# Kernel tuning notes

Hardware: AMD Instinct MI355X
Metric: run time of the kernel (lower is better)

Reference implementation:

```python
import jax, jax.numpy as jnp
import numpy as np
import math

D_MODEL = 1024
N_HEADS = 16
D_K = D_MODEL // N_HEADS
BSZ = 4
SEQ = 2048


def setup_inputs() -> dict:
    key = jax.random.key(0)
    ks = jax.random.split(key, 10)
    x = jax.random.normal(ks[0], (BSZ, SEQ, D_MODEL), dtype=jnp.float32)
    pad_mask = jnp.zeros((BSZ, 1, 1, SEQ), dtype=jnp.int32)
    s = 0.02
    Wq = jax.random.normal(ks[1], (D_MODEL, D_MODEL), jnp.float32) * s
    bq = jax.random.normal(ks[2], (D_MODEL,), jnp.float32) * s
    Wk = jax.random.normal(ks[3], (D_MODEL, D_MODEL), jnp.float32) * s
    bk = jax.random.normal(ks[4], (D_MODEL,), jnp.float32) * s
    Wv = jax.random.normal(ks[5], (D_MODEL, D_MODEL), jnp.float32) * s
    bv = jax.random.normal(ks[6], (D_MODEL,), jnp.float32) * s
    Wo = jax.random.normal(ks[7], (D_MODEL, D_MODEL), jnp.float32) * s
    bo = jax.random.normal(ks[8], (D_MODEL,), jnp.float32) * s
    return {"x": x, "pad_mask": pad_mask, "Wq": Wq, "bq": bq, "Wk": Wk,
            "bk": bk, "Wv": Wv, "bv": bv, "Wo": Wo, "bo": bo}


def reference(x, pad_mask, Wq, bq, Wk, bk, Wv, bv, Wo, bo):
    bsz, seq_len, d_model = x.shape
    h, dk = N_HEADS, D_K

    def split(W, b):
        # torch Linear: x @ W.T + b ; then [b,s,h,dk] -> [b,h,s,dk]
        y = jnp.einsum('bsd,ed->bse', x, W) + b
        return y.reshape(bsz, seq_len, h, dk).transpose(0, 2, 1, 3)

    q = split(Wq, bq)
    k = split(Wk, bk)
    v = split(Wv, bv)

    scores = jnp.einsum('bhqd,bhkd->bhqk', q, k) / math.sqrt(dk)
    causal = jnp.triu(jnp.ones((seq_len, seq_len), dtype=bool), k=1)
    scores = jnp.where(causal[None, None], -jnp.inf, scores)
    scores = jnp.where(pad_mask == 1, -jnp.inf, scores)
    attn = jax.nn.softmax(scores, axis=-1)
    attn = jnp.nan_to_num(attn, nan=0.0)
    out = jnp.einsum('bhqk,bhkd->bhqd', attn, v)
    out = out.transpose(0, 2, 1, 3).reshape(bsz, seq_len, d_model)
    # dropout is identity in eval mode
    return jnp.einsum('bsd,ed->bse', out, Wo) + bo
```

## Files before the change

kernel.cpp:

```cpp
#include <hip/hip_runtime.h>
#include <stdint.h>
#include <stddef.h>


typedef __bf16 bf16;
typedef __bf16 bf16x8 __attribute__((ext_vector_type(8)));
typedef __bf16 bf16x4 __attribute__((ext_vector_type(4)));
typedef float f32x4 __attribute__((ext_vector_type(4)));

#define DM   1024
#define NH   16
#define DK   64
#define BSZ  4
#define SEQL 2048
#define NTOK 8192
#define NEGB -3.0e38f

__device__ __forceinline__ void async16(const bf16* g, void* l) {
  __builtin_amdgcn_global_load_lds(
      (__attribute__((address_space(1))) void*)g,
      (__attribute__((address_space(3))) void*)l, 16, 0, 0);
}

__global__ __launch_bounds__(256) void cvt_all(
    const float* __restrict__ x,
    const float* __restrict__ w0, const float* __restrict__ w1,
    const float* __restrict__ w2, const float* __restrict__ w3,
    const int* __restrict__ pad,
    bf16* __restrict__ xd,
    bf16* __restrict__ d0, bf16* __restrict__ d1,
    bf16* __restrict__ d2, bf16* __restrict__ d3,
    float* __restrict__ padf) {
  int blk = blockIdx.x;
  if (blk >= 6144) {
    int i = (blk - 6144) * 2048 + threadIdx.x * 8;
    int4 p0 = *(const int4*)(pad + i);
    int4 p1 = *(const int4*)(pad + i + 4);
    float4 o0 = {p0.x ? NEGB : 0.f, p0.y ? NEGB : 0.f, p0.z ? NEGB : 0.f, p0.w ? NEGB : 0.f};
    float4 o1 = {p1.x ? NEGB : 0.f, p1.y ? NEGB : 0.f, p1.z ? NEGB : 0.f, p1.w ? NEGB : 0.f};
    *(float4*)(padf + i) = o0;
    *(float4*)(padf + i + 4) = o1;
    return;
  }
  const float* s; bf16* d; int i;
  if (blk < 4096) { s = x; d = xd; i = blk * 2048 + threadIdx.x * 8; }
  else {
    int m = (blk - 4096) >> 9, bi = (blk - 4096) & 511;
    switch (m) {
      case 0:  s = w0; d = d0; break;
      case 1:  s = w1; d = d1; break;
      case 2:  s = w2; d = d2; break;
      default: s = w3; d = d3; break;
    }
    i = bi * 2048 + threadIdx.x * 8;
  }
  float4 v0 = *(const float4*)(s + i);
  float4 v1 = *(const float4*)(s + i + 4);
  bf16x8 o = {(bf16)v0.x, (bf16)v0.y, (bf16)v0.z, (bf16)v0.w,
              (bf16)v1.x, (bf16)v1.y, (bf16)v1.z, (bf16)v1.w};
  *(bf16x8*)(d + i) = o;
}

template <int OUT_MODE>
__device__ __forceinline__ void gemm_core(const bf16* __restrict__ A,
                                          const bf16* __restrict__ W,
                                          const float* __restrict__ bias,
                                          void* __restrict__ outp,
                                          int bm, int bn, char* smem) {
  const int tid  = threadIdx.x;
  const int lane = tid & 63;
  const int wv   = tid >> 6;
  const int wr   = wv >> 2;
  const int wc   = wv & 3;
  const int c    = lane & 15;
  const int quad = lane >> 4;

  const int sr = tid >> 3;
  const int sj = ((tid & 7) ^ (sr & 7)) << 3;
  const bf16* gA = A + (size_t)(bm + sr) * DM + sj;
  const bf16* gB = W + (size_t)(bn + sr) * DM + sj;

#define STAGE_A(TT, TGT) {                                        \
    char* la_ = smem + (TGT) * 49152 + tid * 16;                  \
    async16(gA + (size_t)(TT) * 64, la_);                         \
    async16(gA + (size_t)64 * DM + (size_t)(TT) * 64, la_ + 8192); }
#define STAGE_B(TT, TGT) {                                        \
    char* lb_ = smem + (TGT) * 49152 + 16384 + tid * 16;          \
    async16(gB + (size_t)(TT) * 64, lb_);                         \
    async16(gB + (size_t)64 * DM + (size_t)(TT) * 64, lb_ + 8192);  \
    async16(gB + (size_t)128 * DM + (size_t)(TT) * 64, lb_ + 16384); \
    async16(gB + (size_t)192 * DM + (size_t)(TT) * 64, lb_ + 24576); }

  int aoff[2][4], boff[2][4];
#pragma unroll
  for (int kk = 0; kk < 2; ++kk) {
    const int sw = ((kk * 4 + quad) ^ (c & 7)) << 4;
#pragma unroll
    for (int i = 0; i < 4; ++i) {
      aoff[kk][i] = (wr * 64 + i * 16 + c) * 128 + sw;
      boff[kk][i] = 16384 + (wc * 64 + i * 16 + c) * 128 + sw;
    }
  }

  f32x4 acc[4][4] = {};

  STAGE_A(0, 0) STAGE_B(0, 0)
  STAGE_A(1, 1) STAGE_B(1, 1)
  asm volatile("s_waitcnt vmcnt(6)" ::: "memory");
  __builtin_amdgcn_s_barrier();
  __builtin_amdgcn_sched_barrier(0);

#pragma unroll
  for (int T = 0; T < 16; ++T) {
    const char* bufc = smem + (T % 3) * 49152;
    const int TGT = (T + 2) % 3;
    bf16x8 a0[4], b0[4], a1[4], b1[4];
#pragma unroll
    for (int i = 0; i < 4; ++i) a0[i] = *(const bf16x8*)(bufc + aoff[0][i]);
#pragma unroll
    for (int i = 0; i < 4; ++i) b0[i] = *(const bf16x8*)(bufc + boff[0][i]);
    __builtin_amdgcn_sched_barrier(0);
#pragma unroll
    for (int i = 0; i < 4; ++i) a1[i] = *(const bf16x8*)(bufc + aoff[1][i]);
#pragma unroll
    for (int i = 0; i < 4; ++i) b1[i] = *(const bf16x8*)(bufc + boff[1][i]);
    if (T < 14) { STAGE_A(T + 2, TGT) STAGE_B(T + 2, TGT) }
    __builtin_amdgcn_s_barrier();
    asm volatile("s_waitcnt lgkmcnt(8)" ::: "memory");
    __builtin_amdgcn_sched_barrier(0);
    __builtin_amdgcn_s_setprio(1);
#pragma unroll
    for (int mi = 0; mi < 4; ++mi)
#pragma unroll
      for (int ni = 0; ni < 4; ++ni)
        acc[mi][ni] = __builtin_amdgcn_mfma_f32_16x16x32_bf16(a0[mi], b0[ni],
                                                              acc[mi][ni], 0, 0, 0);
    __builtin_amdgcn_s_setprio(0);
    asm volatile("s_waitcnt lgkmcnt(0)" ::: "memory");
    __builtin_amdgcn_sched_barrier(0);
    __builtin_amdgcn_s_setprio(1);
#pragma unroll
    for (int mi = 0; mi < 4; ++mi)
#pragma unroll
      for (int ni = 0; ni < 4; ++ni)
        acc[mi][ni] = __builtin_amdgcn_mfma_f32_16x16x32_bf16(a1[mi], b1[ni],
                                                              acc[mi][ni], 0, 0, 0);
    __builtin_amdgcn_s_setprio(0);
    if (T < 14)       asm volatile("s_waitcnt vmcnt(6)" ::: "memory");
    else if (T == 14) asm volatile("s_waitcnt vmcnt(0)" ::: "memory");
    __builtin_amdgcn_s_barrier();
    __builtin_amdgcn_sched_barrier(0);
  }
#undef STAGE_A
#undef STAGE_B

  float bias_r[4];
#pragma unroll
  for (int ni = 0; ni < 4; ++ni) bias_r[ni] = bias[bn + wc * 64 + ni * 16 + c];

  if constexpr (OUT_MODE == 2) {
    __syncthreads();
    bf16* vt = (bf16*)smem + wv * 4608;
#pragma unroll
    for (int mi = 0; mi < 4; ++mi)
#pragma unroll
      for (int ni = 0; ni < 4; ++ni) {
        bf16x4 pv = {(bf16)(acc[mi][ni][0] + bias_r[ni]),
                     (bf16)(acc[mi][ni][1] + bias_r[ni]),
                     (bf16)(acc[mi][ni][2] + bias_r[ni]),
                     (bf16)(acc[mi][ni][3] + bias_r[ni])};
        *(bf16x4*)&vt[(ni * 16 + c) * 72 + mi * 16 + quad * 4] = pv;
      }
    const int base = bm + wr * 64;
    const int bb = base >> 11, s0 = base & 2047;
    const int rl = lane >> 3, cl = lane & 7;
#pragma unroll
    for (int it = 0; it < 8; ++it) {
      int d_row = it * 8 + rl;
      bf16x8 v = *(const bf16x8*)&vt[d_row * 72 + cl * 8];
      int n_g = bn + wc * 64 + d_row;
      int hh = n_g >> 6, dd = n_g & 63;
      *(bf16x8*)&((bf16*)outp)[(((size_t)(bb * NH + hh)) * DK + dd) * SEQL + s0 + cl * 8] = v;
    }
    return;
  }

#pragma unroll
  for (int mi = 0; mi < 4; ++mi) {
#pragma unroll
    for (int reg = 0; reg < 4; ++reg) {
      int m_g = bm + wr * 64 + mi * 16 + quad * 4 + reg;
#pragma unroll
      for (int ni = 0; ni < 4; ++ni) {
        int n_g = bn + wc * 64 + ni * 16 + c;
        float v = acc[mi][ni][reg] + bias_r[ni];
        if (OUT_MODE == 0) {
          int b = m_g >> 11, s = m_g & 2047;
          int h = n_g >> 6, d = n_g & 63;
          ((bf16*)outp)[(((size_t)(b * NH + h) * SEQL + s) << 6) + d] = (bf16)v;
        } else {
          ((float*)outp)[(size_t)m_g * DM + n_g] = v;
        }
      }
    }
  }
}

__global__ __launch_bounds__(512, 2) void qkv_gemm(
    const bf16* __restrict__ X,
    const bf16* __restrict__ Wq, const bf16* __restrict__ Wk, const bf16* __restrict__ Wv,
    const float* __restrict__ bq, const float* __restrict__ bk, const float* __restrict__ bv,
    bf16* __restrict__ Q, bf16* __restrict__ K, bf16* __restrict__ Vt) {
  __shared__ alignas(16) char smem[147456];
  const int f = blockIdx.x;
  const int wg = (f & 7) * 96 + (f >> 3);
  const int y = wg / 12, t = wg % 12;
  const int z = t >> 2, x = t & 3;
  const int bm = y * 128, bn = x * 256;
  if (z < 2)
    gemm_core<0>(X, z ? Wk : Wq, z ? bk : bq, z ? (void*)K : (void*)Q, bm, bn, smem);
  else
    gemm_core<2>(X, Wv, bv, Vt, bm, bn, smem);
}

__global__ __launch_bounds__(512, 2) void out_gemm(const bf16* __restrict__ A,
                                                   const bf16* __restrict__ W,
                                                   const float* __restrict__ bias,
                                                   float* __restrict__ out) {
  __shared__ alignas(16) char smem[147456];
  const int f = blockIdx.x;
  const int wg = (f & 7) * 32 + (f >> 3);
  gemm_core<1>(A, W, bias, out, (wg >> 2) * 128, (wg & 3) * 256, smem);
}

__global__ __launch_bounds__(512, 2) void attn_kernel(
    const bf16* __restrict__ Q, const bf16* __restrict__ K,
    const bf16* __restrict__ Vt, const float* __restrict__ padf,
    bf16* __restrict__ O) {
  const int B = blockIdx.x;
  const int bh = (B & 7) + 8 * (B >> 5);
  const int t  = (B >> 3) & 3;
  const int b = bh >> 4, h = bh & 15;
  const int tid  = threadIdx.x;
  const int lane = tid & 63;
  const int wv   = tid >> 6;
  const int c    = lane & 15;
  const int quad = lane >> 4;

  __shared__ bf16 Ks[2][64 * 64];
  __shared__ bf16 Vs[2][64 * 64];
  __shared__ bf16 Pl_all[8][32 * 64];
  bf16* Pl = &Pl_all[wv][0];

  const bf16* Qh  = Q  + (size_t)bh * SEQL * DK;
  const bf16* Kh  = K  + (size_t)bh * SEQL * DK;
  const bf16* Vth = Vt + (size_t)bh * DK * SEQL;
  const float* pb = padf + b * SEQL;

  const int sr = tid >> 3;
  const int sj = ((tid & 7) ^ (sr & 7)) * 8;
  const bf16* gK = Kh  + (size_t)sr * DK   + sj;
  const bf16* gV = Vth + (size_t)sr * SEQL + sj;
  bf16* lK0 = &Ks[0][tid * 8]; bf16* lK1 = &Ks[1][tid * 8];
  bf16* lV0 = &Vs[0][tid * 8]; bf16* lV1 = &Vs[1][tid * 8];

  const float sc = 0.1803368801111204f;

  for (int pass = 0; pass < 2; ++pass) {
    const int qt  = pass ? 7 - t : t;
    const int R   = qt * 256 + wv * 32;
    const int nkt = (qt + 1) * 4;

    bf16x8 Qf[2][2];
#pragma unroll
    for (int qg = 0; qg < 2; ++qg)
#pragma unroll
      for (int kh = 0; kh < 2; ++kh)
        Qf[qg][kh] = *(const bf16x8*)&Qh[(size_t)(R + qg * 16 + c) * DK + kh * 32 + quad * 8];

    f32x4 Oc[2][4] = {};
    float ls[2] = {0.f, 0.f};

    __syncthreads();
    async16(gK, lK0);
    async16(gV, lV0);

    for (int kt = 0; kt < nkt; ++kt) {
      const int cur = kt & 1;
      const int kb = kt * 64;
      __syncthreads();

      if (kt + 1 < nkt) {
        async16(gK + (size_t)(kt + 1) * 64 * DK, cur ? lK0 : lK1);
        async16(gV + (size_t)(kt + 1) * 64,      cur ? lV0 : lV1);
      }
      if (kb > R + 31) continue;

      float4 bc[4];
#pragma unroll
      for (int kf = 0; kf < 4; ++kf)
        bc[kf] = *(const float4*)&pb[kb + kf * 16 + quad * 4];

      const bf16* Kc = cur ? Ks[1] : Ks[0];
      const bf16* Vc = cur ? Vs[1] : Vs[0];

      bf16x8 Kf[4][2], Vf[4][2];
#pragma unroll
      for (int kf = 0; kf < 4; ++kf)
#pragma unroll
        for (int kh = 0; kh < 2; ++kh)
          Kf[kf][kh] = *(const bf16x8*)&Kc[(kf * 16 + c) * 64 + (((kh * 4 + quad) ^ (c & 7)) * 8)];
#pragma unroll
      for (int df = 0; df < 4; ++df)
#pragma unroll
        for (int kv = 0; kv < 2; ++kv)
          Vf[df][kv] = *(const bf16x8*)&Vc[(df * 16 + c) * 64 + (((kv * 4 + quad) ^ (c & 7)) * 8)];

      f32x4 st[2][4] = {};
#pragma unroll
      for (int qg = 0; qg < 2; ++qg)
#pragma unroll
        for (int kh = 0; kh < 2; ++kh)
#pragma unroll
          for (int kf = 0; kf < 4; ++kf)
            st[qg][kf] = __builtin_amdgcn_mfma_f32_16x16x32_bf16(Kf[kf][kh], Qf[qg][kh],
                                                                 st[qg][kf], 0, 0, 0);

      const bool dg = (kb + 63 > R);
#pragma unroll
      for (int qg = 0; qg < 2; ++qg) {
        const int qrow = R + qg * 16 + c;
#pragma unroll
        for (int kf = 0; kf < 4; ++kf) {
          const float* bv4 = (const float*)&bc[kf];
          float p4[4];
#pragma unroll
          for (int r = 0; r < 4; ++r) {
            float e = __builtin_amdgcn_exp2f(__builtin_fmaf(st[qg][kf][r], sc, bv4[r]));
            if (dg && (kb + kf * 16 + quad * 4 + r > qrow)) e = 0.f;
            p4[r] = e;
            ls[qg] += e;
          }
          bf16x4 pk = {(bf16)p4[0], (bf16)p4[1], (bf16)p4[2], (bf16)p4[3]};
          *(bf16x4*)&Pl[(qg * 16 + c) * 64 +
                        (((kf * 2 + (quad >> 1)) ^ (c & 7)) * 8) + (quad & 1) * 4] = pk;
        }
      }

#pragma unroll
      for (int qg = 0; qg < 2; ++qg)
#pragma unroll
        for (int kv = 0; kv < 2; ++kv) {
          bf16x8 af = *(const bf16x8*)&Pl[(qg * 16 + c) * 64 +
                                          (((kv * 4 + quad) ^ (c & 7)) * 8)];
#pragma unroll
          for (int df = 0; df < 4; ++df)
            Oc[qg][df] = __builtin_amdgcn_mfma_f32_16x16x32_bf16(af, Vf[df][kv],
                                                                 Oc[qg][df], 0, 0, 0);
        }
    }

#pragma unroll
    for (int qg = 0; qg < 2; ++qg) {
      float l = ls[qg];
      l += __shfl_xor(l, 16);
      l += __shfl_xor(l, 32);
      float linv = (l > 0.f) ? 1.f / l : 0.f;
      float lr[4];
#pragma unroll
      for (int r = 0; r < 4; ++r) lr[r] = __shfl(linv, quad * 4 + r);
#pragma unroll
      for (int r = 0; r < 4; ++r) {
        size_t row = (size_t)(b * SEQL + R + qg * 16 + quad * 4 + r) * DM + h * DK;
#pragma unroll
        for (int df = 0; df < 4; ++df)
          O[row + df * 16 + c] = (bf16)(Oc[qg][df][r] * lr[r]);
      }
    }
  }
}

extern "C" void kernel_launch(void* const* d_in, const int* in_sizes, int n_in,
                              void* d_out, int out_size, void* d_ws, size_t ws_size,
                              hipStream_t stream) {
  const float* x   = (const float*)d_in[0];
  const int*   pad = (const int*)d_in[1];
  const float* Wq  = (const float*)d_in[2];
  const float* bq  = (const float*)d_in[3];
  const float* Wk  = (const float*)d_in[4];
  const float* bk  = (const float*)d_in[5];
  const float* Wv  = (const float*)d_in[6];
  const float* bv  = (const float*)d_in[7];
  const float* Wo  = (const float*)d_in[8];
  const float* bo  = (const float*)d_in[9];
  float* out = (float*)d_out;

  const size_t SZ_X = (size_t)NTOK * DM * 2;
  const size_t SZ_W = (size_t)DM * DM * 2;
  char* ws = (char*)d_ws;
  bf16* Xb  = (bf16*)ws;  ws += SZ_X;
  bf16* Wqb = (bf16*)ws;  ws += SZ_W;
  bf16* Wkb = (bf16*)ws;  ws += SZ_W;
  bf16* Wvb = (bf16*)ws;  ws += SZ_W;
  bf16* Wob = (bf16*)ws;  ws += SZ_W;
  bf16* Qb  = (bf16*)ws;  ws += SZ_X;
  bf16* Kb  = (bf16*)ws;  ws += SZ_X;
  bf16* Vtb = (bf16*)ws;  ws += SZ_X;
  bf16* Ob  = (bf16*)ws;  ws += SZ_X;
  float* padfb = (float*)ws; ws += (size_t)NTOK * 4;

  cvt_all<<<6148, 256, 0, stream>>>(x, Wq, Wk, Wv, Wo, pad,
                                    Xb, Wqb, Wkb, Wvb, Wob, padfb);
  qkv_gemm<<<768, 512, 0, stream>>>(Xb, Wqb, Wkb, Wvb, bq, bk, bv, Qb, Kb, Vtb);
  attn_kernel<<<256, 512, 0, stream>>>(Qb, Kb, Vtb, padfb, Ob);
  out_gemm<<<256, 512, 0, stream>>>(Ob, Wob, bo, out);
}
```

Baseline: 251.5 us.

## Rework GEMM core into BK=32 four-stage pipeline with 256-row tiles for QKV

Replaces the 3-stage, K=64 GEMM pipeline with a 4-stage, K=32 pipeline templated on the M tile size. The QKV projection now uses 256x256 tiles, halving the grid to 384 blocks, and splits each K step into two MFMA halves with staggered B staging. The aim is more reuse per tile and finer-grained overlap of global-to-LDS loads with compute. The cost is more barriers per K step, a larger accumulator that adds register pressure, and fewer blocks to balance across CUs.

After: 246.5 us. 1.02x faster.

```diff
diff --git a/kernel.cpp b/kernel.cpp
--- a/kernel.cpp
+++ b/kernel.cpp
@@ -61,12 +61,14 @@
   *(bf16x8*)(d + i) = o;
 }
 
-template <int OUT_MODE>
-__device__ __forceinline__ void gemm_core(const bf16* __restrict__ A,
+template <int BM, int OUT_MODE>
+__device__ __forceinline__ void gemm_fine(const bf16* __restrict__ A,
                                           const bf16* __restrict__ W,
                                           const float* __restrict__ bias,
                                           void* __restrict__ outp,
                                           int bm, int bn, char* smem) {
+  constexpr int MFR  = BM / 32;
+  constexpr int ABUF = BM * 64;
   const int tid  = threadIdx.x;
   const int lane = tid & 63;
   const int wv   = tid >> 6;
@@ -75,67 +77,54 @@
   const int c    = lane & 15;
   const int quad = lane >> 4;
 
-  const int sr = tid >> 3;
-  const int sj = ((tid & 7) ^ (sr & 7)) << 3;
-  const bf16* gA = A + (size_t)(bm + sr) * DM + sj;
-  const bf16* gB = W + (size_t)(bn + sr) * DM + sj;
-
-#define STAGE_A(TT, TGT) {                                        \
-    char* la_ = smem + (TGT) * 49152 + tid * 16;                  \
-    async16(gA + (size_t)(TT) * 64, la_);                         \
-    async16(gA + (size_t)64 * DM + (size_t)(TT) * 64, la_ + 8192); }
-#define STAGE_B(TT, TGT) {                                        \
-    char* lb_ = smem + (TGT) * 49152 + 16384 + tid * 16;          \
-    async16(gB + (size_t)(TT) * 64, lb_);                         \
-    async16(gB + (size_t)64 * DM + (size_t)(TT) * 64, lb_ + 8192);  \
-    async16(gB + (size_t)128 * DM + (size_t)(TT) * 64, lb_ + 16384); \
-    async16(gB + (size_t)192 * DM + (size_t)(TT) * 64, lb_ + 24576); }
-
-  int aoff[2][4], boff[2][4];
-#pragma unroll
-  for (int kk = 0; kk < 2; ++kk) {
-    const int sw = ((kk * 4 + quad) ^ (c & 7)) << 4;
-#pragma unroll
-    for (int i = 0; i < 4; ++i) {
-      aoff[kk][i] = (wr * 64 + i * 16 + c) * 128 + sw;
-      boff[kk][i] = 16384 + (wc * 64 + i * 16 + c) * 128 + sw;
-    }
-  }
-
-  f32x4 acc[4][4] = {};
-
-  STAGE_A(0, 0) STAGE_B(0, 0)
-  STAGE_A(1, 1) STAGE_B(1, 1)
-  asm volatile("s_waitcnt vmcnt(6)" ::: "memory");
+  char* Ab4 = smem;
+  char* Bb4 = smem + 4 * ABUF;
+
+  const int sr  = tid >> 2;
+  const int sjj = ((tid & 3) ^ (sr & 3)) * 8;
+  const bf16* gA = A + (size_t)(bm + sr) * DM + sjj;
+  const bf16* gB = W + (size_t)(bn + sr) * DM + sjj;
+
+#define STG_A(KT, U) {                                                   \
+    char* la_ = Ab4 + (U) * ABUF + tid * 16;                             \
+    async16(gA + (size_t)(KT) * 32, la_);                                \
+    if constexpr (BM == 256)                                             \
+      async16(gA + (size_t)(KT) * 32 + (size_t)128 * DM, la_ + 8192); }
+#define STG_B(KT, U) {                                                   \
+    char* lb_ = Bb4 + (U) * 16384 + tid * 16;                            \
+    async16(gB + (size_t)(KT) * 32, lb_);                                \
+    async16(gB + (size_t)(KT) * 32 + (size_t)128 * DM, lb_ + 8192); }
+
+  const int sw = (quad ^ (c & 3)) * 16;
+  int aoff[MFR], boff[4];
+#pragma unroll
+  for (int i = 0; i < MFR; ++i) aoff[i] = (wr * (BM / 2) + i * 16 + c) * 64 + sw;
+#pragma unroll
+  for (int i = 0; i < 4; ++i)   boff[i] = (wc * 64 + i * 16 + c) * 64 + sw;
+
+  f32x4 acc[MFR][4] = {};
+
+  STG_A(0, 0) STG_B(0, 0)
+  STG_A(1, 1) STG_B(1, 1)
+  STG_A(2, 2) STG_B(2, 2)
+  if constexpr (BM == 256) asm volatile("s_waitcnt vmcnt(8)" ::: "memory");
+  else                     asm volatile("s_waitcnt vmcnt(6)" ::: "memory");
   __builtin_amdgcn_s_barrier();
   __builtin_amdgcn_sched_barrier(0);
 
 #pragma unroll
-  for (int T = 0; T < 16; ++T) {
-    const char* bufc = smem + (T % 3) * 49152;
-    const int TGT = (T + 2) % 3;
-    bf16x8 a0[4], b0[4], a1[4], b1[4];
-#pragma unroll
-    for (int i = 0; i < 4; ++i) a0[i] = *(const bf16x8*)(bufc + aoff[0][i]);
-#pragma unroll
-    for (int i = 0; i < 4; ++i) b0[i] = *(const bf16x8*)(bufc + boff[0][i]);
-    __builtin_amdgcn_sched_barrier(0);
-#pragma unroll
-    for (int i = 0; i < 4; ++i) a1[i] = *(const bf16x8*)(bufc + aoff[1][i]);
-#pragma unroll
-    for (int i = 0; i < 4; ++i) b1[i] = *(const bf16x8*)(bufc + boff[1][i]);
-    if (T < 14) { STAGE_A(T + 2, TGT) STAGE_B(T + 2, TGT) }
+  for (int kt = 0; kt < 32; ++kt) {
+    const char* Ac = Ab4 + (kt & 3) * ABUF;
+    const char* Bc = Bb4 + (kt & 3) * 16384;
+    const int u = (kt + 3) & 3;
+    bf16x8 a[4], b[4];
+#pragma unroll
+    for (int i = 0; i < 4; ++i) a[i] = *(const bf16x8*)(Ac + aoff[i]);
+#pragma unroll
+    for (int i = 0; i < 4; ++i) b[i] = *(const bf16x8*)(Bc + boff[i]);
+    if (kt + 3 < 32) STG_A(kt + 3, u)
+    if constexpr (BM == 128) { if (kt + 3 < 32) STG_B(kt + 3, u) }
     __builtin_amdgcn_s_barrier();
-    asm volatile("s_waitcnt lgkmcnt(8)" ::: "memory");
-    __builtin_amdgcn_sched_barrier(0);
-    __builtin_amdgcn_s_setprio(1);
-#pragma unroll
-    for (int mi = 0; mi < 4; ++mi)
-#pragma unroll
-      for (int ni = 0; ni < 4; ++ni)
-        acc[mi][ni] = __builtin_amdgcn_mfma_f32_16x16x32_bf16(a0[mi], b0[ni],
-                                                              acc[mi][ni], 0, 0, 0);
-    __builtin_amdgcn_s_setprio(0);
     asm volatile("s_waitcnt lgkmcnt(0)" ::: "memory");
     __builtin_amdgcn_sched_barrier(0);
     __builtin_amdgcn_s_setprio(1);
@@ -143,16 +132,42 @@
     for (int mi = 0; mi < 4; ++mi)
 #pragma unroll
       for (int ni = 0; ni < 4; ++ni)
-        acc[mi][ni] = __builtin_amdgcn_mfma_f32_16x16x32_bf16(a1[mi], b1[ni],
+        acc[mi][ni] = __builtin_amdgcn_mfma_f32_16x16x32_bf16(a[mi], b[ni],
                                                               acc[mi][ni], 0, 0, 0);
     __builtin_amdgcn_s_setprio(0);
-    if (T < 14)       asm volatile("s_waitcnt vmcnt(6)" ::: "memory");
-    else if (T == 14) asm volatile("s_waitcnt vmcnt(0)" ::: "memory");
-    __builtin_amdgcn_s_barrier();
-    __builtin_amdgcn_sched_barrier(0);
-  }
-#undef STAGE_A
-#undef STAGE_B
+    if constexpr (BM == 256) {
+      __builtin_amdgcn_s_barrier();
+#pragma unroll
+      for (int i = 0; i < 4; ++i) a[i] = *(const bf16x8*)(Ac + aoff[4 + i]);
+      if (kt + 3 < 32) STG_B(kt + 3, u)
+      __builtin_amdgcn_s_barrier();
+      asm volatile("s_waitcnt lgkmcnt(0)" ::: "memory");
+      __builtin_amdgcn_sched_barrier(0);
+      __builtin_amdgcn_s_setprio(1);
+#pragma unroll
+      for (int mi = 0; mi < 4; ++mi)
+#pragma unroll
+        for (int ni = 0; ni < 4; ++ni)
+          acc[4 + mi][ni] = __builtin_amdgcn_mfma_f32_16x16x32_bf16(a[mi], b[ni],
+                                                                    acc[4 + mi][ni], 0, 0, 0);
+      __builtin_amdgcn_s_setprio(0);
+    }
+    if (kt < 29) {
+      if constexpr (BM == 256) asm volatile("s_waitcnt vmcnt(8)" ::: "memory");
+      else                     asm volatile("s_waitcnt vmcnt(6)" ::: "memory");
+    } else if (kt == 29) {
+      if constexpr (BM == 256) asm volatile("s_waitcnt vmcnt(4)" ::: "memory");
+      else                     asm volatile("s_waitcnt vmcnt(3)" ::: "memory");
+    } else if (kt == 30) {
+      asm volatile("s_waitcnt vmcnt(0)" ::: "memory");
+    }
+    if (kt != 31) {
+      __builtin_amdgcn_s_barrier();
+      __builtin_amdgcn_sched_barrier(0);
+    }
+  }
+#undef STG_A
+#undef STG_B
 
   float bias_r[4];
 #pragma unroll
@@ -162,39 +177,41 @@
     __syncthreads();
     bf16* vt = (bf16*)smem + wv * 4608;
 #pragma unroll
-    for (int mi = 0; mi < 4; ++mi)
-#pragma unroll
-      for (int ni = 0; ni < 4; ++ni) {
-        bf16x4 pv = {(bf16)(acc[mi][ni][0] + bias_r[ni]),
-                     (bf16)(acc[mi][ni][1] + bias_r[ni]),
-                     (bf16)(acc[mi][ni][2] + bias_r[ni]),
-                     (bf16)(acc[mi][ni][3] + bias_r[ni])};
-        *(bf16x4*)&vt[(ni * 16 + c) * 72 + mi * 16 + quad * 4] = pv;
+    for (int mh = 0; mh < 2; ++mh) {
+#pragma unroll
+      for (int mi = 0; mi < 4; ++mi)
+#pragma unroll
+        for (int ni = 0; ni < 4; ++ni) {
+          f32x4 av = acc[mh * 4 + mi][ni];
+          bf16x4 pv = {(bf16)(av[0] + bias_r[ni]), (bf16)(av[1] + bias_r[ni]),
+                       (bf16)(av[2] + bias_r[ni]), (bf16)(av[3] + bias_r[ni])};
+          *(bf16x4*)&vt[(ni * 16 + c) * 72 + mi * 16 + quad * 4] = pv;
+        }
+      const int base = bm + wr * 128 + mh * 64;
+      const int bb = base >> 11, s0 = base & 2047;
+      const int rl = lane >> 3, cl = lane & 7;
+#pragma unroll
+      for (int it = 0; it < 8; ++it) {
+        int d_row = it * 8 + rl;
+        bf16x8 v = *(const bf16x8*)&vt[d_row * 72 + cl * 8];
+        int n_g = bn + wc * 64 + d_row;
+        int hh = n_g >> 6, dd = n_g & 63;
+        *(bf16x8*)&((bf16*)outp)[(((size_t)(bb * NH + hh)) * DK + dd) * SEQL + s0 + cl * 8] = v;
       }
-    const int base = bm + wr * 64;
-    const int bb = base >> 11, s0 = base & 2047;
-    const int rl = lane >> 3, cl = lane & 7;
-#pragma unroll
-    for (int it = 0; it < 8; ++it) {
-      int d_row = it * 8 + rl;
-      bf16x8 v = *(const bf16x8*)&vt[d_row * 72 + cl * 8];
-      int n_g = bn + wc * 64 + d_row;
-      int hh = n_g >> 6, dd = n_g & 63;
-      *(bf16x8*)&((bf16*)outp)[(((size_t)(bb * NH + hh)) * DK + dd) * SEQL + s0 + cl * 8] = v;
     }
     return;
   }
 
 #pragma unroll
-  for (int mi = 0; mi < 4; ++mi) {
+  for (int mi = 0; mi < MFR; ++mi) {
 #pragma unroll
     for (int reg = 0; reg < 4; ++reg) {
-      int m_g = bm + wr * 64 + mi * 16 + quad * 4 + reg;
+      int m_g = bm + wr * (BM / 2) + mi * 16 + quad * 4 + reg;
 #pragma unroll
       for (int ni = 0; ni < 4; ++ni) {
         int n_g = bn + wc * 64 + ni * 16 + c;
         float v = acc[mi][ni][reg] + bias_r[ni];
-        if (OUT_MODE == 0) {
+        if constexpr (OUT_MODE == 0) {
           int b = m_g >> 11, s = m_g & 2047;
           int h = n_g >> 6, d = n_g & 63;
           ((bf16*)outp)[(((size_t)(b * NH + h) * SEQL + s) << 6) + d] = (bf16)v;
@@ -211,26 +228,27 @@
     const bf16* __restrict__ Wq, const bf16* __restrict__ Wk, const bf16* __restrict__ Wv,
     const float* __restrict__ bq, const float* __restrict__ bk, const float* __restrict__ bv,
     bf16* __restrict__ Q, bf16* __restrict__ K, bf16* __restrict__ Vt) {
-  __shared__ alignas(16) char smem[147456];
+  __shared__ alignas(16) char smem[131072];
   const int f = blockIdx.x;
-  const int wg = (f & 7) * 96 + (f >> 3);
-  const int y = wg / 12, t = wg % 12;
-  const int z = t >> 2, x = t & 3;
-  const int bm = y * 128, bn = x * 256;
-  if (z < 2)
-    gemm_core<0>(X, z ? Wk : Wq, z ? bk : bq, z ? (void*)K : (void*)Q, bm, bn, smem);
-  else
-    gemm_core<2>(X, Wv, bv, Vt, bm, bn, smem);
+  const int l = f >> 3;
+  const int np  = l / 12;
+  const int rem = l % 12;
+  const int z   = rem >> 2;
+  const int mp  = (f & 7) * 4 + (rem & 3);
+  const int bm = mp * 256, bn = np * 256;
+  if (z == 0)      gemm_fine<256, 0>(X, Wq, bq, Q,  bm, bn, smem);
+  else if (z == 1) gemm_fine<256, 0>(X, Wk, bk, K,  bm, bn, smem);
+  else             gemm_fine<256, 2>(X, Wv, bv, Vt, bm, bn, smem);
 }
 
 __global__ __launch_bounds__(512, 2) void out_gemm(const bf16* __restrict__ A,
                                                    const bf16* __restrict__ W,
                                                    const float* __restrict__ bias,
                                                    float* __restrict__ out) {
-  __shared__ alignas(16) char smem[147456];
+  __shared__ alignas(16) char smem[98304];
   const int f = blockIdx.x;
   const int wg = (f & 7) * 32 + (f >> 3);
-  gemm_core<1>(A, W, bias, out, (wg >> 2) * 128, (wg & 3) * 256, smem);
+  gemm_fine<128, 1>(A, W, bias, out, (wg >> 2) * 128, (wg & 3) * 256, smem);
 }
 
 __global__ __launch_bounds__(512, 2) void attn_kernel(
@@ -411,7 +429,7 @@
 
   cvt_all<<<6148, 256, 0, stream>>>(x, Wq, Wk, Wv, Wo, pad,
                                     Xb, Wqb, Wkb, Wvb, Wob, padfb);
-  qkv_gemm<<<768, 512, 0, stream>>>(Xb, Wqb, Wkb, Wvb, bq, bk, bv, Qb, Kb, Vtb);
+  qkv_gemm<<<384, 512, 0, stream>>>(Xb, Wqb, Wkb, Wvb, bq, bk, bv, Qb, Kb, Vtb);
   attn_kernel<<<256, 512, 0, stream>>>(Qb, Kb, Vtb, padfb, Ob);
   out_gemm<<<256, 512, 0, stream>>>(Ob, Wob, bo, out);
 }
```

## Halve GEMM K-tile to cut LDS footprint and raise occupancy

Applied to the files above, without the earlier changes.

The shared GEMM core now stages 32-wide K slices instead of 64-wide ones. It keeps a 3-deep async LDS ring, which shrinks LDS use from 144KB to 72KB per block, and raises launch bounds to 4 waves per SIMD so more blocks fit per CU. Block-to-tile mapping is also changed so each XCD gets a contiguous set of M rows, aiming at better L2 reuse of activations. The cost is twice as many barrier-separated iterations with less MFMA work between each, and register pressure under the tighter launch bound may cause spills.

Result: faster. 235.0 us (-6.5%).

```diff
diff --git a/kernel.cpp b/kernel.cpp
--- a/kernel.cpp
+++ b/kernel.cpp
@@ -62,7 +62,7 @@
 }
 
 template <int OUT_MODE>
-__device__ __forceinline__ void gemm_core(const bf16* __restrict__ A,
+__device__ __forceinline__ void gemm_fine(const bf16* __restrict__ A,
                                           const bf16* __restrict__ W,
                                           const float* __restrict__ bias,
                                           void* __restrict__ outp,
@@ -75,67 +75,46 @@
   const int c    = lane & 15;
   const int quad = lane >> 4;
 
-  const int sr = tid >> 3;
-  const int sj = ((tid & 7) ^ (sr & 7)) << 3;
-  const bf16* gA = A + (size_t)(bm + sr) * DM + sj;
-  const bf16* gB = W + (size_t)(bn + sr) * DM + sj;
-
-#define STAGE_A(TT, TGT) {                                        \
-    char* la_ = smem + (TGT) * 49152 + tid * 16;                  \
-    async16(gA + (size_t)(TT) * 64, la_);                         \
-    async16(gA + (size_t)64 * DM + (size_t)(TT) * 64, la_ + 8192); }
-#define STAGE_B(TT, TGT) {                                        \
-    char* lb_ = smem + (TGT) * 49152 + 16384 + tid * 16;          \
-    async16(gB + (size_t)(TT) * 64, lb_);                         \
-    async16(gB + (size_t)64 * DM + (size_t)(TT) * 64, lb_ + 8192);  \
-    async16(gB + (size_t)128 * DM + (size_t)(TT) * 64, lb_ + 16384); \
-    async16(gB + (size_t)192 * DM + (size_t)(TT) * 64, lb_ + 24576); }
-
-  int aoff[2][4], boff[2][4];
-#pragma unroll
-  for (int kk = 0; kk < 2; ++kk) {
-    const int sw = ((kk * 4 + quad) ^ (c & 7)) << 4;
-#pragma unroll
-    for (int i = 0; i < 4; ++i) {
-      aoff[kk][i] = (wr * 64 + i * 16 + c) * 128 + sw;
-      boff[kk][i] = 16384 + (wc * 64 + i * 16 + c) * 128 + sw;
-    }
+  char* Ab = smem;
+  char* Bb = smem + 24576;
+
+  const int sr  = tid >> 2;
+  const int sjj = ((tid & 3) ^ (sr & 3)) * 8;
+  const bf16* gA = A + (size_t)(bm + sr) * DM + sjj;
+  const bf16* gB = W + (size_t)(bn + sr) * DM + sjj;
+
+#define STG(KT, U) {                                                     \
+    async16(gA + (size_t)(KT) * 32, Ab + (U) * 8192 + tid * 16);         \
+    async16(gB + (size_t)(KT) * 32, Bb + (U) * 16384 + tid * 16);        \
+    async16(gB + (size_t)(KT) * 32 + (size_t)128 * DM,                   \
+            Bb + (U) * 16384 + 8192 + tid * 16); }
+
+  const int sw = (quad ^ (c & 3)) * 16;
+  int aoff[4], boff[4];
+#pragma unroll
+  for (int i = 0; i < 4; ++i) {
+    aoff[i] = (wr * 64 + i * 16 + c) * 64 + sw;
+    boff[i] = (wc * 64 + i * 16 + c) * 64 + sw;
   }
 
   f32x4 acc[4][4] = {};
 
-  STAGE_A(0, 0) STAGE_B(0, 0)
-  STAGE_A(1, 1) STAGE_B(1, 1)
-  asm volatile("s_waitcnt vmcnt(6)" ::: "memory");
+  STG(0, 0) STG(1, 1)
+  asm volatile("s_waitcnt vmcnt(3)" ::: "memory");
   __builtin_amdgcn_s_barrier();
   __builtin_amdgcn_sched_barrier(0);
 
 #pragma unroll
-  for (int T = 0; T < 16; ++T) {
-    const char* bufc = smem + (T % 3) * 49152;
-    const int TGT = (T + 2) % 3;
-    bf16x8 a0[4], b0[4], a1[4], b1[4];
-#pragma unroll
-    for (int i = 0; i < 4; ++i) a0[i] = *(const bf16x8*)(bufc + aoff[0][i]);
-#pragma unroll
-    for (int i = 0; i < 4; ++i) b0[i] = *(const bf16x8*)(bufc + boff[0][i]);
-    __builtin_amdgcn_sched_barrier(0);
-#pragma unroll
-    for (int i = 0; i < 4; ++i) a1[i] = *(const bf16x8*)(bufc + aoff[1][i]);
-#pragma unroll
-    for (int i = 0; i < 4; ++i) b1[i] = *(const bf16x8*)(bufc + boff[1][i]);
-    if (T < 14) { STAGE_A(T + 2, TGT) STAGE_B(T + 2, TGT) }
+  for (int kt = 0; kt < 32; ++kt) {
+    const char* Ac = Ab + (kt % 3) * 8192;
+    const char* Bc = Bb + (kt % 3) * 16384;
+    bf16x8 a[4], b[4];
+#pragma unroll
+    for (int i = 0; i < 4; ++i) a[i] = *(const bf16x8*)(Ac + aoff[i]);
+#pragma unroll
+    for (int i = 0; i < 4; ++i) b[i] = *(const bf16x8*)(Bc + boff[i]);
+    if (kt + 2 < 32) STG(kt + 2, (kt + 2) % 3)
     __builtin_amdgcn_s_barrier();
-    asm volatile("s_waitcnt lgkmcnt(8)" ::: "memory");
-    __builtin_amdgcn_sched_barrier(0);
-    __builtin_amdgcn_s_setprio(1);
-#pragma unroll
-    for (int mi = 0; mi < 4; ++mi)
-#pragma unroll
-      for (int ni = 0; ni < 4; ++ni)
-        acc[mi][ni] = __builtin_amdgcn_mfma_f32_16x16x32_bf16(a0[mi], b0[ni],
-                                                              acc[mi][ni], 0, 0, 0);
-    __builtin_amdgcn_s_setprio(0);
     asm volatile("s_waitcnt lgkmcnt(0)" ::: "memory");
     __builtin_amdgcn_sched_barrier(0);
     __builtin_amdgcn_s_setprio(1);
@@ -143,16 +122,17 @@
     for (int mi = 0; mi < 4; ++mi)
 #pragma unroll
       for (int ni = 0; ni < 4; ++ni)
-        acc[mi][ni] = __builtin_amdgcn_mfma_f32_16x16x32_bf16(a1[mi], b1[ni],
+        acc[mi][ni] = __builtin_amdgcn_mfma_f32_16x16x32_bf16(a[mi], b[ni],
                                                               acc[mi][ni], 0, 0, 0);
     __builtin_amdgcn_s_setprio(0);
-    if (T < 14)       asm volatile("s_waitcnt vmcnt(6)" ::: "memory");
-    else if (T == 14) asm volatile("s_waitcnt vmcnt(0)" ::: "memory");
-    __builtin_amdgcn_s_barrier();
-    __builtin_amdgcn_sched_barrier(0);
-  }
-#undef STAGE_A
-#undef STAGE_B
+    if (kt <= 29)      asm volatile("s_waitcnt vmcnt(3)" ::: "memory");
+    else if (kt == 30) asm volatile("s_waitcnt vmcnt(0)" ::: "memory");
+    if (kt != 31) {
+      __builtin_amdgcn_s_barrier();
+      __builtin_amdgcn_sched_barrier(0);
+    }
+  }
+#undef STG
 
   float bias_r[4];
 #pragma unroll
@@ -194,7 +174,7 @@
       for (int ni = 0; ni < 4; ++ni) {
         int n_g = bn + wc * 64 + ni * 16 + c;
         float v = acc[mi][ni][reg] + bias_r[ni];
-        if (OUT_MODE == 0) {
+        if constexpr (OUT_MODE == 0) {
           int b = m_g >> 11, s = m_g & 2047;
           int h = n_g >> 6, d = n_g & 63;
           ((bf16*)outp)[(((size_t)(b * NH + h) * SEQL + s) << 6) + d] = (bf16)v;
@@ -206,31 +186,34 @@
   }
 }
 
-__global__ __launch_bounds__(512, 2) void qkv_gemm(
+__global__ __launch_bounds__(512, 4) void qkv_gemm(
     const bf16* __restrict__ X,
     const bf16* __restrict__ Wq, const bf16* __restrict__ Wk, const bf16* __restrict__ Wv,
     const float* __restrict__ bq, const float* __restrict__ bk, const float* __restrict__ bv,
     bf16* __restrict__ Q, bf16* __restrict__ K, bf16* __restrict__ Vt) {
-  __shared__ alignas(16) char smem[147456];
-  const int f = blockIdx.x;
-  const int wg = (f & 7) * 96 + (f >> 3);
-  const int y = wg / 12, t = wg % 12;
-  const int z = t >> 2, x = t & 3;
-  const int bm = y * 128, bn = x * 256;
-  if (z < 2)
-    gemm_core<0>(X, z ? Wk : Wq, z ? bk : bq, z ? (void*)K : (void*)Q, bm, bn, smem);
-  else
-    gemm_core<2>(X, Wv, bv, Vt, bm, bn, smem);
-}
-
-__global__ __launch_bounds__(512, 2) void out_gemm(const bf16* __restrict__ A,
+  __shared__ alignas(16) char smem[73728];
+  const int f   = blockIdx.x;
+  const int xcd = f & 7;
+  const int c96 = f >> 3;
+  const int z   = c96 >> 5;
+  const int r   = c96 & 31;
+  const int bm  = (xcd * 8 + (r >> 2)) * 128;
+  const int bn  = (r & 3) * 256;
+  if (z == 0)      gemm_fine<0>(X, Wq, bq, Q,  bm, bn, smem);
+  else if (z == 1) gemm_fine<0>(X, Wk, bk, K,  bm, bn, smem);
+  else             gemm_fine<2>(X, Wv, bv, Vt, bm, bn, smem);
+}
+
+__global__ __launch_bounds__(512, 4) void out_gemm(const bf16* __restrict__ A,
                                                    const bf16* __restrict__ W,
                                                    const float* __restrict__ bias,
                                                    float* __restrict__ out) {
-  __shared__ alignas(16) char smem[147456];
-  const int f = blockIdx.x;
-  const int wg = (f & 7) * 32 + (f >> 3);
-  gemm_core<1>(A, W, bias, out, (wg >> 2) * 128, (wg & 3) * 256, smem);
+  __shared__ alignas(16) char smem[73728];
+  const int f   = blockIdx.x;
+  const int c32 = f >> 3;
+  const int bm  = ((f & 7) * 8 + (c32 >> 2)) * 128;
+  const int bn  = (c32 & 3) * 256;
+  gemm_fine<1>(A, W, bias, out, bm, bn, smem);
 }
 
 __global__ __launch_bounds__(512, 2) void attn_kernel(
```
